# Optimization experiments

Hardware: AMD Instinct MI355X
Metric: run time of the kernel (lower is better)

## Reference

```python
import jax, jax.numpy as jnp
import numpy as np

N_TOKENS = 2048
HIDDEN = 2880
N_HEADS = 64          # total query heads
N_KV = 8              # key/value heads
Q_MULT = N_HEADS // N_KV
HEAD_DIM = 64
SLIDING_WINDOW = 128  # layer_idx=0 -> sliding-window layer
SM_SCALE = 1.0 / np.sqrt(HEAD_DIM)
RMS_EPS = 1e-5
ROPE_BASE = 150000.0
ROPE_SCALING = 32.0
INIT_CTX = 4096
NTK_ALPHA = 1.0
NTK_BETA = 32.0


def _rope_tables(num_tokens):
    # YaRN NTK-by-parts inverse frequencies (static constants)
    freq = ROPE_BASE ** (np.arange(0, HEAD_DIM, 2, dtype=np.float64) / HEAD_DIM)
    concentration = 0.1 * np.log(ROPE_SCALING) + 1.0
    d_half = HEAD_DIM / 2
    low = d_half * np.log(INIT_CTX / (NTK_BETA * 2 * np.pi)) / np.log(ROPE_BASE)
    high = d_half * np.log(INIT_CTX / (NTK_ALPHA * 2 * np.pi)) / np.log(ROPE_BASE)
    interpolation = 1.0 / (ROPE_SCALING * freq)
    extrapolation = 1.0 / freq
    ramp = (np.arange(d_half) - low) / (high - low)
    m = 1.0 - np.clip(ramp, 0.0, 1.0)
    inv_freq = interpolation * (1.0 - m) + extrapolation * m
    t = np.arange(num_tokens, dtype=np.float64)
    freqs = np.outer(t, inv_freq)
    cos = jnp.asarray((np.cos(freqs) * concentration), dtype=jnp.float32)
    sin = jnp.asarray((np.sin(freqs) * concentration), dtype=jnp.float32)
    return cos, sin  # [num_tokens, HEAD_DIM//2]


def _apply_rotary(x, cos, sin):
    # x: [n, heads, HEAD_DIM]
    c = cos[:, None, :].astype(x.dtype)
    s = sin[:, None, :].astype(x.dtype)
    x1, x2 = jnp.split(x, 2, axis=-1)
    return jnp.concatenate([x1 * c - x2 * s, x2 * c + x1 * s], axis=-1)


def setup_inputs() -> dict:
    key = jax.random.key(0)
    ks = jax.random.split(key, 7)
    return {
        "x": jax.random.normal(ks[0], (N_TOKENS, HIDDEN), jnp.float32),
        "scale": jax.random.uniform(ks[1], (HIDDEN,), jnp.float32, 0.5, 1.5),
        "sink": jax.random.normal(ks[2], (N_HEADS,), jnp.float32),
        "w_qkv": jax.random.normal(ks[3], (HIDDEN, (N_HEADS + 2 * N_KV) * HEAD_DIM), jnp.float32) * 0.02,
        "b_qkv": jax.random.normal(ks[4], ((N_HEADS + 2 * N_KV) * HEAD_DIM,), jnp.float32) * 0.02,
        "w_o": jax.random.normal(ks[5], (N_HEADS * HEAD_DIM, HIDDEN), jnp.float32) * 0.02,
        "b_o": jax.random.normal(ks[6], (HIDDEN,), jnp.float32) * 0.02,
    }


def reference(x, scale, sink, w_qkv, b_qkv, w_o, b_o):
    n = x.shape[0]
    # RMSNorm (fp32)
    t = x.astype(jnp.float32)
    rms = jnp.sqrt(jnp.mean(t * t, axis=-1, keepdims=True) + RMS_EPS)
    t = (t / rms) * scale

    # QKV projection + split
    qkv = t @ w_qkv + b_qkv
    q_sz = N_HEADS * HEAD_DIM
    kv_sz = N_KV * HEAD_DIM
    q = qkv[:, :q_sz].reshape(n, N_HEADS, HEAD_DIM)
    k = qkv[:, q_sz:q_sz + kv_sz].reshape(n, N_KV, HEAD_DIM)
    v = qkv[:, q_sz + kv_sz:].reshape(n, N_KV, HEAD_DIM)

    # RoPE (YaRN)
    cos, sin = _rope_tables(n)
    q = _apply_rotary(q, cos, sin)
    k = _apply_rotary(k, cos, sin)

    # GQA layout: [n, N_KV, Q_MULT, HEAD_DIM]
    qg = q.reshape(n, N_KV, Q_MULT, HEAD_DIM)

    # scores: [N_KV, Q_MULT, n_q, n_kv]
    scores = jnp.einsum('nhgd,mhd->hgnm', qg, k) * SM_SCALE

    # causal + sliding-window mask
    q_pos = jnp.arange(n)[:, None]
    kv_pos = jnp.arange(n)[None, :]
    mask = jnp.where(kv_pos > q_pos, -jnp.inf, 0.0)
    mask = mask + jnp.where((SLIDING_WINDOW > 0) & (q_pos - kv_pos > SLIDING_WINDOW), -jnp.inf, 0.0)
    scores = scores + mask[None, None, :, :].astype(scores.dtype)

    # sink logit appended as extra softmax column, then dropped
    s_col = jnp.broadcast_to(sink.reshape(N_KV, Q_MULT, 1, 1), (N_KV, Q_MULT, n, 1))
    w = jax.nn.softmax(jnp.concatenate([scores, s_col], axis=-1), axis=-1)[..., :-1]

    attn = jnp.einsum('hgnm,mhd->nhgd', w, v).reshape(n, N_HEADS * HEAD_DIM)
    out = attn @ w_o + b_o
    return x + out


if __name__ == '__main__':
    inp = setup_inputs()
    y = reference(**inp)
    print(y.shape, y.dtype)
```

## Files before the change

kernel.cpp:

```cpp
#include <hip/hip_runtime.h>
#include <cstdint>
#include <cstddef>

#define HIDDEN   2880
#define QKV_N    5120
#define OPROJ_K  4096
#define NTOK     2048
#define WIN      128
#define SM_SCALE 0.125f

typedef _Float16 half8  __attribute__((ext_vector_type(8)));
typedef _Float16 half4v __attribute__((ext_vector_type(4)));
typedef float    f32x4  __attribute__((ext_vector_type(4)));

__device__ __forceinline__ void gload16(const void* g, void* l) {
  __builtin_amdgcn_global_load_lds((__attribute__((address_space(1))) void*)g,
                                   (__attribute__((address_space(3))) void*)l,
                                   16, 0, 0);
}

__device__ __forceinline__ _Float16 f2h(float f) { return (_Float16)f; }

__global__ __launch_bounds__(256) void rmsnorm_kernel(const float* __restrict__ x,
                                                      const float* __restrict__ scale,
                                                      _Float16* __restrict__ out) {
  int row = blockIdx.x, t = threadIdx.x;
  const float4* xr = (const float4*)(x + (size_t)row * HIDDEN);
  const float4* sc = (const float4*)scale;
  float4 v0 = xr[t];
  float4 v1 = xr[t + 256];
  float4 v2 = (t < 208) ? xr[t + 512] : make_float4(0.f, 0.f, 0.f, 0.f);
  float ss = v0.x*v0.x + v0.y*v0.y + v0.z*v0.z + v0.w*v0.w
           + v1.x*v1.x + v1.y*v1.y + v1.z*v1.z + v1.w*v1.w
           + v2.x*v2.x + v2.y*v2.y + v2.z*v2.z + v2.w*v2.w;
  #pragma unroll
  for (int m = 1; m < 64; m <<= 1) ss += __shfl_xor(ss, m, 64);
  __shared__ float red[4];
  if ((t & 63) == 0) red[t >> 6] = ss;
  __syncthreads();
  float inv = 1.0f / sqrtf((red[0] + red[1] + red[2] + red[3]) * (1.0f / HIDDEN) + 1e-5f);
  _Float16* orow = out + (size_t)row * HIDDEN;
  auto store4 = [&](int c4, const float4& v, const float4& s) {
    half4v h;
    h[0] = f2h(v.x * inv * s.x); h[1] = f2h(v.y * inv * s.y);
    h[2] = f2h(v.z * inv * s.z); h[3] = f2h(v.w * inv * s.w);
    *(half4v*)(orow + (size_t)c4 * 4) = h;
  };
  store4(t, v0, sc[t]);
  store4(t + 256, v1, sc[t + 256]);
  if (t < 208) store4(t + 512, v2, sc[t + 512]);
}

__global__ __launch_bounds__(256) void cast_transpose_kernel(const float* __restrict__ W,
                                                             _Float16* __restrict__ Wt,
                                                             int K, int N) {
  __shared__ float tile[32][33];
  int n0 = blockIdx.x * 32, k0 = blockIdx.y * 32;
  int t = threadIdx.x;
  #pragma unroll
  for (int p = 0; p < 4; ++p) {
    int e = t + p * 256; int r = e >> 5, cc = e & 31;
    float vv = 0.f;
    if (n0 + cc < N) vv = W[(size_t)(k0 + r) * N + n0 + cc];
    tile[r][cc] = vv;
  }
  __syncthreads();
  #pragma unroll
  for (int p = 0; p < 4; ++p) {
    int e = t + p * 256; int r = e >> 5, cc = e & 31;
    Wt[(size_t)(n0 + r) * K + k0 + cc] = (_Float16)tile[cc][r];
  }
}

template <bool HALF_OUT>
__global__ __launch_bounds__(256, 2) void gemm_kernel(const _Float16* __restrict__ A,
                                                      const _Float16* __restrict__ Bt,
                                                      const float* __restrict__ bias,
                                                      const float* __restrict__ resid,
                                                      void* __restrict__ Cout,
                                                      int M, int N, int K) {
  __shared__ _Float16 Alds[128 * 32];
  __shared__ _Float16 Blds[128 * 32];
  int tid = threadIdx.x;
  int wave = tid >> 6, lane = tid & 63;
  int wm = wave >> 1, wn = wave & 1;
  int c = lane & 15, quad = lane >> 4;
  int m0 = blockIdx.y * 128, n0 = blockIdx.x * 128;

  int c0 = wave * 128 + lane;
  const _Float16* gA0 = A  + (size_t)(m0 + (c0 >> 2)) * K + (c0 & 3) * 8;
  const _Float16* gA1 = A  + (size_t)(m0 + ((c0 + 64) >> 2)) * K + (c0 & 3) * 8;
  const _Float16* gB0 = Bt + (size_t)(n0 + (c0 >> 2)) * K + (c0 & 3) * 8;
  const _Float16* gB1 = Bt + (size_t)(n0 + ((c0 + 64) >> 2)) * K + (c0 & 3) * 8;
  _Float16* lA0 = Alds + wave * 1024;
  _Float16* lA1 = lA0 + 512;
  _Float16* lB0 = Blds + wave * 1024;
  _Float16* lB1 = lB0 + 512;

  f32x4 acc[4][4] = {};
  int nIter = K >> 5;
  for (int kt = 0; kt < nIter; ++kt) {
    __syncthreads();
    gload16(gA0, lA0); gload16(gA1, lA1);
    gload16(gB0, lB0); gload16(gB1, lB1);
    gA0 += 32; gA1 += 32; gB0 += 32; gB1 += 32;
    __syncthreads();
    half8 a[4], b[4];
    #pragma unroll
    for (int i = 0; i < 4; ++i)
      a[i] = *(const half8*)&Alds[(wm * 64 + i * 16 + c) * 32 + quad * 8];
    #pragma unroll
    for (int j = 0; j < 4; ++j)
      b[j] = *(const half8*)&Blds[(wn * 64 + j * 16 + c) * 32 + quad * 8];
    #pragma unroll
    for (int i = 0; i < 4; ++i)
      #pragma unroll
      for (int j = 0; j < 4; ++j)
        acc[i][j] = __builtin_amdgcn_mfma_f32_16x16x32_f16(a[i], b[j], acc[i][j], 0, 0, 0);
  }

  #pragma unroll
  for (int i = 0; i < 4; ++i) {
    int row = m0 + wm * 64 + i * 16 + quad * 4;
    #pragma unroll
    for (int j = 0; j < 4; ++j) {
      int col = n0 + wn * 64 + j * 16 + c;
      if (col < N) {
        float bv = bias[col];
        #pragma unroll
        for (int r = 0; r < 4; ++r) {
          float v = acc[i][j][r] + bv;
          if (resid) v += resid[(size_t)(row + r) * N + col];
          if (HALF_OUT) ((_Float16*)Cout)[(size_t)(row + r) * N + col] = f2h(v);
          else          ((float*)Cout)[(size_t)(row + r) * N + col] = v;
        }
      }
    }
  }
}

__global__ __launch_bounds__(256) void rope_kernel(const _Float16* __restrict__ qkv,
                                                   _Float16* __restrict__ qh,
                                                   _Float16* __restrict__ kh,
                                                   _Float16* __restrict__ vh) {
  int tok = blockIdx.x, t = threadIdx.x;
  __shared__ float cs[32], sn[32];
  if (t < 32) {
    const double PI = 3.14159265358979323846;
    double i = (double)t;
    double lf = log(150000.0);
    double freq = exp(lf * (i / 32.0));
    double interp = 1.0 / (32.0 * freq);
    double extrap = 1.0 / freq;
    double low  = 32.0 * log(4096.0 / (32.0 * 2.0 * PI)) / lf;
    double high = 32.0 * log(4096.0 / (2.0 * PI)) / lf;
    double ramp = (i - low) / (high - low);
    double mm = 1.0 - fmin(fmax(ramp, 0.0), 1.0);
    double invf = interp * (1.0 - mm) + extrap * mm;
    double ang = (double)tok * invf;
    double conc = 0.1 * log(32.0) + 1.0;
    cs[t] = (float)(cos(ang) * conc);
    sn[t] = (float)(sin(ang) * conc);
  }
  __syncthreads();
  const _Float16* row = qkv + (size_t)tok * QKV_N;
  #pragma unroll
  for (int p = 0; p < 8; ++p) {
    int pid = t + p * 256;
    int hh = pid >> 5, d = pid & 31;
    float x1 = (float)row[hh * 64 + d], x2 = (float)row[hh * 64 + d + 32];
    float cv = cs[d], sv = sn[d];
    _Float16* dst = qh + ((size_t)tok * 64 + hh) * 64 + d;
    dst[0]  = f2h(x1 * cv - x2 * sv);
    dst[32] = f2h(x2 * cv + x1 * sv);
  }
  {
    int hh = t >> 5, d = t & 31;
    float x1 = (float)row[4096 + hh * 64 + d], x2 = (float)row[4096 + hh * 64 + d + 32];
    float cv = cs[d], sv = sn[d];
    _Float16* dst = kh + ((size_t)tok * 8 + hh) * 64 + d;
    dst[0]  = f2h(x1 * cv - x2 * sv);
    dst[32] = f2h(x2 * cv + x1 * sv);
  }
  #pragma unroll
  for (int p = 0; p < 2; ++p) {
    int idx = t + p * 256;
    vh[(size_t)tok * 512 + idx] = row[4608 + idx];
  }
}

#define TQ 16
__global__ __launch_bounds__(256) void attn_kernel(const _Float16* __restrict__ qh,
                                                   const _Float16* __restrict__ kh,
                                                   const _Float16* __restrict__ vh,
                                                   const float* __restrict__ sink,
                                                   _Float16* __restrict__ attn_out) {
  __shared__ _Float16 Vt[64 * 160];
  __shared__ _Float16 Ps[128 * 160];
  int qt = blockIdx.x, kvh = blockIdx.y;
  int Q0 = qt * TQ;
  int kmin = (Q0 >= WIN) ? Q0 - WIN : 0;
  int nkv = Q0 + TQ - kmin;
  int tid = threadIdx.x;
  int wave = tid >> 6, lane = tid & 63;
  int c = lane & 15, quad = lane >> 4;

  #pragma unroll
  for (int p = 0; p < 5; ++p) {
    int cc = p * 256 + tid;
    int col = cc % 160;
    int d0 = (cc / 160) * 8;
    union { uint4 u4; _Float16 hv[8]; } buf;
    if (col < nkv) buf.u4 = *(const uint4*)(vh + ((size_t)(kmin + col) * 8 + kvh) * 64 + d0);
    else           buf.u4 = make_uint4(0, 0, 0, 0);
    #pragma unroll
    for (int uu = 0; uu < 8; ++uu) Vt[(d0 + uu) * 160 + col] = buf.hv[uu];
  }
  #pragma unroll
  for (int p = 0; p < 8; ++p) {
    int idx = p * 256 + tid;
    Ps[(idx >> 4) * 160 + 144 + (idx & 15)] = (_Float16)0.f;
  }

  half8 aq[2][2];
  #pragma unroll
  for (int i = 0; i < 2; ++i) {
    int qm = wave * 2 + i;
    #pragma unroll
    for (int ks = 0; ks < 2; ++ks)
      aq[i][ks] = *(const half8*)(qh + ((size_t)(Q0 + c) * 64 + kvh * 8 + qm) * 64 + ks * 32 + quad * 8);
  }

  f32x4 sacc[2][9] = {};
  #pragma unroll
  for (int j = 0; j < 9; ++j) {
    #pragma unroll
    for (int ks = 0; ks < 2; ++ks) {
      half8 bk = *(const half8*)(kh + ((size_t)(kmin + j * 16 + c) * 8 + kvh) * 64 + ks * 32 + quad * 8);
      #pragma unroll
      for (int i = 0; i < 2; ++i)
        sacc[i][j] = __builtin_amdgcn_mfma_f32_16x16x32_f16(aq[i][ks], bk, sacc[i][j], 0, 0, 0);
    }
  }

  #pragma unroll
  for (int i = 0; i < 2; ++i) {
    int qm = wave * 2 + i;
    float sk = sink[kvh * 8 + qm];
    #pragma unroll
    for (int r = 0; r < 4; ++r) {
      int qpos = Q0 + quad * 4 + r;
      float sv[9]; float mx = -3e38f;
      #pragma unroll
      for (int j = 0; j < 9; ++j) {
        int key = kmin + j * 16 + c;
        float s = sacc[i][j][r] * SM_SCALE;
        bool valid = (key <= qpos) && (qpos - key <= WIN);
        sv[j] = valid ? s : -3e38f;
        mx = fmaxf(mx, sv[j]);
      }
      #pragma unroll
      for (int msk = 1; msk < 16; msk <<= 1) mx = fmaxf(mx, __shfl_xor(mx, msk, 64));
      mx = fmaxf(mx, sk);
      float sum = 0.f; float pv[9];
      #pragma unroll
      for (int j = 0; j < 9; ++j) { float p = __expf(sv[j] - mx); pv[j] = p; sum += p; }
      #pragma unroll
      for (int msk = 1; msk < 16; msk <<= 1) sum += __shfl_xor(sum, msk, 64);
      sum += __expf(sk - mx);
      float inv = 1.0f / sum;
      int mrow = qm * 16 + quad * 4 + r;
      #pragma unroll
      for (int j = 0; j < 9; ++j)
        Ps[mrow * 160 + j * 16 + c] = f2h(pv[j] * inv);
    }
  }

  __syncthreads();

  f32x4 oacc[2][4] = {};
  #pragma unroll
  for (int ks = 0; ks < 5; ++ks) {
    half8 ap[2], bv[4];
    #pragma unroll
    for (int i = 0; i < 2; ++i)
      ap[i] = *(const half8*)&Ps[((wave * 2 + i) * 16 + c) * 160 + ks * 32 + quad * 8];
    #pragma unroll
    for (int j = 0; j < 4; ++j)
      bv[j] = *(const half8*)&Vt[(j * 16 + c) * 160 + ks * 32 + quad * 8];
    #pragma unroll
    for (int i = 0; i < 2; ++i)
      #pragma unroll
      for (int j = 0; j < 4; ++j)
        oacc[i][j] = __builtin_amdgcn_mfma_f32_16x16x32_f16(ap[i], bv[j], oacc[i][j], 0, 0, 0);
  }

  #pragma unroll
  for (int i = 0; i < 2; ++i) {
    int qm = wave * 2 + i;
    #pragma unroll
    for (int j = 0; j < 4; ++j)
      #pragma unroll
      for (int r = 0; r < 4; ++r) {
        int token = Q0 + quad * 4 + r;
        attn_out[(size_t)token * 4096 + (kvh * 8 + qm) * 64 + j * 16 + c] = f2h(oacc[i][j][r]);
      }
  }
}

extern "C" void kernel_launch(void* const* d_in, const int* in_sizes, int n_in,
                              void* d_out, int out_size, void* d_ws, size_t ws_size,
                              hipStream_t stream) {
  (void)in_sizes; (void)n_in; (void)out_size; (void)ws_size;
  const float* x      = (const float*)d_in[0];
  const float* scale  = (const float*)d_in[1];
  const float* sink   = (const float*)d_in[2];
  const float* w_qkv  = (const float*)d_in[3];
  const float* b_qkv  = (const float*)d_in[4];
  const float* w_o    = (const float*)d_in[5];
  const float* b_o    = (const float*)d_in[6];
  float* out = (float*)d_out;

  char* ws = (char*)d_ws;
  size_t off = 0;
  auto alloc = [&](size_t bytes) { void* p = ws + off; off += (bytes + 255) & ~(size_t)255; return p; };
  _Float16* a_h   = (_Float16*)alloc((size_t)NTOK * HIDDEN * 2);
  _Float16* wtq   = (_Float16*)alloc((size_t)QKV_N * HIDDEN * 2);
  _Float16* wto   = (_Float16*)alloc((size_t)2944 * OPROJ_K * 2);
  _Float16* qkv_h = (_Float16*)alloc((size_t)NTOK * QKV_N * 2);
  _Float16* q_h   = (_Float16*)alloc((size_t)NTOK * 4096 * 2);
  _Float16* k_h   = (_Float16*)alloc((size_t)NTOK * 512 * 2);
  _Float16* v_h   = (_Float16*)alloc((size_t)NTOK * 512 * 2);
  _Float16* at_h  = (_Float16*)alloc((size_t)NTOK * 4096 * 2);

  cast_transpose_kernel<<<dim3(QKV_N / 32, HIDDEN / 32), 256, 0, stream>>>(w_qkv, wtq, HIDDEN, QKV_N);
  cast_transpose_kernel<<<dim3(2944 / 32, OPROJ_K / 32), 256, 0, stream>>>(w_o, wto, OPROJ_K, HIDDEN);
  rmsnorm_kernel<<<NTOK, 256, 0, stream>>>(x, scale, a_h);
  gemm_kernel<true><<<dim3(QKV_N / 128, NTOK / 128), 256, 0, stream>>>(
      a_h, wtq, b_qkv, nullptr, qkv_h, NTOK, QKV_N, HIDDEN);
  rope_kernel<<<NTOK, 256, 0, stream>>>(qkv_h, q_h, k_h, v_h);
  attn_kernel<<<dim3(NTOK / TQ, 8), 256, 0, stream>>>(q_h, k_h, v_h, sink, at_h);
  gemm_kernel<false><<<dim3(23, NTOK / 128), 256, 0, stream>>>(
      at_h, wto, b_o, x, out, NTOK, HIDDEN, OPROJ_K);
}
```

Baseline: 405.1 us.

## Shrink GEMM M-tile to 64, swizzle LDS layout, vectorize transpose stores

Templates the GEMM on its M-tile size and launches both projections with 64-row tiles, doubling the grid so the GPU's compute units are better filled, and raises the launch-bounds occupancy hint to 4 blocks. An XOR swizzle on the k-chunk index is applied consistently to the async global-to-LDS loads and to the fragment reads, to cut LDS bank conflicts. The cast-transpose kernel now writes four halves per thread as one vector store. Smaller tiles lower per-block reuse of the B operand and raise global traffic for it.

```diff
diff --git a/kernel.cpp b/kernel.cpp
--- a/kernel.cpp
+++ b/kernel.cpp
@@ -65,63 +65,82 @@
     tile[r][cc] = vv;
   }
   __syncthreads();
-  #pragma unroll
-  for (int p = 0; p < 4; ++p) {
-    int e = t + p * 256; int r = e >> 5, cc = e & 31;
-    Wt[(size_t)(n0 + r) * K + k0 + cc] = (_Float16)tile[cc][r];
-  }
-}
-
-template <bool HALF_OUT>
-__global__ __launch_bounds__(256, 2) void gemm_kernel(const _Float16* __restrict__ A,
+  {
+    int r = t >> 3, c4 = (t & 7) * 4;
+    half4v h;
+    #pragma unroll
+    for (int u = 0; u < 4; ++u) h[u] = (_Float16)tile[c4 + u][r];
+    *(half4v*)&Wt[(size_t)(n0 + r) * K + k0 + c4] = h;
+  }
+}
+
+template <int BM, bool HALF_OUT>
+__global__ __launch_bounds__(256, 4) void gemm_kernel(const _Float16* __restrict__ A,
                                                       const _Float16* __restrict__ Bt,
                                                       const float* __restrict__ bias,
                                                       const float* __restrict__ resid,
                                                       void* __restrict__ Cout,
                                                       int M, int N, int K) {
-  __shared__ _Float16 Alds[128 * 32];
+  constexpr int MI = BM / 32;
+  constexpr int NA = (BM * 4) / 256;
+  __shared__ _Float16 Alds[BM * 32];
   __shared__ _Float16 Blds[128 * 32];
   int tid = threadIdx.x;
   int wave = tid >> 6, lane = tid & 63;
   int wm = wave >> 1, wn = wave & 1;
   int c = lane & 15, quad = lane >> 4;
-  int m0 = blockIdx.y * 128, n0 = blockIdx.x * 128;
-
-  int c0 = wave * 128 + lane;
-  const _Float16* gA0 = A  + (size_t)(m0 + (c0 >> 2)) * K + (c0 & 3) * 8;
-  const _Float16* gA1 = A  + (size_t)(m0 + ((c0 + 64) >> 2)) * K + (c0 & 3) * 8;
-  const _Float16* gB0 = Bt + (size_t)(n0 + (c0 >> 2)) * K + (c0 & 3) * 8;
-  const _Float16* gB1 = Bt + (size_t)(n0 + ((c0 + 64) >> 2)) * K + (c0 & 3) * 8;
-  _Float16* lA0 = Alds + wave * 1024;
-  _Float16* lA1 = lA0 + 512;
-  _Float16* lB0 = Blds + wave * 1024;
-  _Float16* lB1 = lB0 + 512;
-
-  f32x4 acc[4][4] = {};
+  int m0 = blockIdx.y * BM, n0 = blockIdx.x * 128;
+
+  const _Float16* gAp[NA]; _Float16* lAp[NA];
+  #pragma unroll
+  for (int i = 0; i < NA; ++i) {
+    int p = wave * 64 + i * 256 + lane;
+    int r = p >> 2;
+    int lk = (p & 3) ^ ((r >> 1) & 3);
+    gAp[i] = A + (size_t)(m0 + r) * K + lk * 8;
+    lAp[i] = Alds + (size_t)(wave * 64 + i * 256) * 8;
+  }
+  const _Float16* gBp[2]; _Float16* lBp[2];
+  #pragma unroll
+  for (int i = 0; i < 2; ++i) {
+    int p = wave * 64 + i * 256 + lane;
+    int r = p >> 2;
+    int lk = (p & 3) ^ ((r >> 1) & 3);
+    gBp[i] = Bt + (size_t)(n0 + r) * K + lk * 8;
+    lBp[i] = Blds + (size_t)(wave * 64 + i * 256) * 8;
+  }
+
+  int phys8 = (quad ^ ((c >> 1) & 3)) * 8;
+  f32x4 acc[MI][4] = {};
   int nIter = K >> 5;
   for (int kt = 0; kt < nIter; ++kt) {
     __syncthreads();
-    gload16(gA0, lA0); gload16(gA1, lA1);
-    gload16(gB0, lB0); gload16(gB1, lB1);
-    gA0 += 32; gA1 += 32; gB0 += 32; gB1 += 32;
+    #pragma unroll
+    for (int i = 0; i < NA; ++i) { gload16(gAp[i], lAp[i]); gAp[i] += 32; }
+    #pragma unroll
+    for (int i = 0; i < 2; ++i)  { gload16(gBp[i], lBp[i]); gBp[i] += 32; }
     __syncthreads();
-    half8 a[4], b[4];
-    #pragma unroll
-    for (int i = 0; i < 4; ++i)
-      a[i] = *(const half8*)&Alds[(wm * 64 + i * 16 + c) * 32 + quad * 8];
-    #pragma unroll
-    for (int j = 0; j < 4; ++j)
-      b[j] = *(const half8*)&Blds[(wn * 64 + j * 16 + c) * 32 + quad * 8];
-    #pragma unroll
-    for (int i = 0; i < 4; ++i)
+    half8 a[MI], b[4];
+    #pragma unroll
+    for (int i = 0; i < MI; ++i) {
+      int row = wm * (BM / 2) + i * 16 + c;
+      a[i] = *(const half8*)&Alds[row * 32 + phys8];
+    }
+    #pragma unroll
+    for (int j = 0; j < 4; ++j) {
+      int row = wn * 64 + j * 16 + c;
+      b[j] = *(const half8*)&Blds[row * 32 + phys8];
+    }
+    #pragma unroll
+    for (int i = 0; i < MI; ++i)
       #pragma unroll
       for (int j = 0; j < 4; ++j)
         acc[i][j] = __builtin_amdgcn_mfma_f32_16x16x32_f16(a[i], b[j], acc[i][j], 0, 0, 0);
   }
 
   #pragma unroll
-  for (int i = 0; i < 4; ++i) {
-    int row = m0 + wm * 64 + i * 16 + quad * 4;
+  for (int i = 0; i < MI; ++i) {
+    int row = m0 + wm * (BM / 2) + i * 16 + quad * 4;
     #pragma unroll
     for (int j = 0; j < 4; ++j) {
       int col = n0 + wn * 64 + j * 16 + c;
@@ -336,10 +355,10 @@
   cast_transpose_kernel<<<dim3(QKV_N / 32, HIDDEN / 32), 256, 0, stream>>>(w_qkv, wtq, HIDDEN, QKV_N);
   cast_transpose_kernel<<<dim3(2944 / 32, OPROJ_K / 32), 256, 0, stream>>>(w_o, wto, OPROJ_K, HIDDEN);
   rmsnorm_kernel<<<NTOK, 256, 0, stream>>>(x, scale, a_h);
-  gemm_kernel<true><<<dim3(QKV_N / 128, NTOK / 128), 256, 0, stream>>>(
+  gemm_kernel<64, true><<<dim3(QKV_N / 128, NTOK / 64), 256, 0, stream>>>(
       a_h, wtq, b_qkv, nullptr, qkv_h, NTOK, QKV_N, HIDDEN);
   rope_kernel<<<NTOK, 256, 0, stream>>>(qkv_h, q_h, k_h, v_h);
   attn_kernel<<<dim3(NTOK / TQ, 8), 256, 0, stream>>>(q_h, k_h, v_h, sink, at_h);
-  gemm_kernel<false><<<dim3(23, NTOK / 128), 256, 0, stream>>>(
+  gemm_kernel<64, false><<<dim3(23, NTOK / 64), 256, 0, stream>>>(
       at_h, wto, b_o, x, out, NTOK, HIDDEN, OPROJ_K);
 }
```

Result: slower. 417.4 us (+3.0%).
